# Performance work log

Hardware: AMD Instinct MI355X
Metric: run time of the kernel (lower is better)

Reference implementation:

```python
import jax, jax.numpy as jnp
import numpy as np

N_NODES = 100000
N_EDGES = 1600000
IN_DIM = 128
HID = 128
OUT_DIM = 64
EPS = 1e-8


def setup_inputs() -> dict:
    key = jax.random.key(0)
    ks = jax.random.split(key, 10)
    x = jax.random.normal(ks[0], (N_NODES, IN_DIM), dtype=jnp.float32)
    edge_index = jax.random.randint(ks[1], (2, N_EDGES), 0, N_NODES, dtype=jnp.int64)
    edge_attr = jax.random.uniform(ks[2], (N_EDGES, 4), dtype=jnp.float32)
    s1 = 1.0 / np.sqrt(IN_DIM)
    s2 = 1.0 / np.sqrt(HID)
    sr = 1.0 / np.sqrt(2 * HID)
    W1 = jax.random.normal(ks[3], (HID, IN_DIM), dtype=jnp.float32) * s1
    b1 = jnp.zeros((HID,), dtype=jnp.float32)
    W2 = jax.random.normal(ks[4], (HID, HID), dtype=jnp.float32) * s2
    b2 = jnp.zeros((HID,), dtype=jnp.float32)
    Wr = jax.random.normal(ks[5], (OUT_DIM, 2 * HID), dtype=jnp.float32) * sr
    br = jnp.zeros((OUT_DIM,), dtype=jnp.float32)
    return {"x": x, "edge_index": edge_index, "edge_attr": edge_attr,
            "W1": W1, "b1": b1, "W2": W2, "b2": b2, "Wr": Wr, "br": br}


def _edge_weight_from_attr_auto(edge_attr):
    # mean over features, min-max normalize, invert, clamp >= 0
    m = edge_attr.mean(axis=-1)                      # [E]
    m_min, m_max = m.min(), m.max()
    m_norm = (m - m_min) / (m_max - m_min + EPS)
    w = jnp.where(m_max - m_min > EPS, 1.0 - m_norm, jnp.ones_like(m))
    return jnp.clip(w, 0.0)


def reference(x, edge_index, edge_attr, W1, b1, W2, b2, Wr, br):
    N = x.shape[0]
    row, col = edge_index[0], edge_index[1]          # source -> target
    ew = _edge_weight_from_attr_auto(edge_attr)      # [E]
    # GCN normalization with self-loops (self-loop weight = 1.0)
    deg = jax.ops.segment_sum(ew, col, num_segments=N) + 1.0   # [N]
    dis = jax.lax.rsqrt(deg)                         # deg >= 1
    norm = dis[row] * ew * dis[col]                  # [E]

    def gcn(h, W, b):
        hW = h @ W.T                                 # [N, d_out]
        agg = jax.ops.segment_sum(norm[:, None] * hW[row], col, num_segments=N)
        # self-loop contribution: dis[i] * 1.0 * dis[i] * hW[i]
        return agg + (dis * dis)[:, None] * hW + b

    # dropout in eval mode -> identity
    h1 = jax.nn.relu(gcn(x, W1, b1))                 # [N, HID]
    h2 = jax.nn.relu(gcn(h1, W2, b2))                # [N, HID]
    hcat = jnp.concatenate([h1, h2], axis=-1)        # [N, 2*HID] (JK concat)
    return hcat @ Wr.T + br                          # residue-level [N, OUT_DIM]
```

## Files before the change

### kernel.cpp

```cpp
#include <hip/hip_runtime.h>

#define NN 100000
#define NE 1600000
#define HID 128
#define ODIM 64
#define NBK 196
#define BSHIFT 9
#define BGRID 512
#define CVTB 48
#define CHUNK 3125
#define BITER 13
#define BINCAP 12288
#define SMAX 4504
#define LMAX 568

typedef unsigned int u32;
typedef unsigned short u16;
typedef __bf16 bf16x8 __attribute__((ext_vector_type(8)));
typedef float f32x4 __attribute__((ext_vector_type(4)));
typedef float f32x2 __attribute__((ext_vector_type(2)));

__device__ __forceinline__ float bf_lo(u32 p){ return __uint_as_float(p << 16); }
__device__ __forceinline__ float bf_hi(u32 p){ return __uint_as_float(p & 0xffff0000u); }
__device__ __forceinline__ u16 f2bf(float f){
  u32 u = __float_as_uint(f);
  u += 0x7fffu + ((u >> 16) & 1u);
  return (u16)(u >> 16);
}
__device__ __forceinline__ bf16x8 ld8bf(const u16* p){ return *(const bf16x8*)p; }
__device__ __forceinline__ bf16x8 cvt8(const float* p){
  union { bf16x8 v; u16 s[8]; } r;
#pragma unroll
  for (int i = 0; i < 8; i++) r.s[i] = f2bf(p[i]);
  return r.v;
}

__global__ __launch_bounds__(256) void k_bin(
    const float* __restrict__ eattr, const int* __restrict__ erow,
    const int* __restrict__ ecol, u32* __restrict__ bcur,
    uint2* __restrict__ bin, u32* __restrict__ minmax,
    const float* __restrict__ W1, const float* __restrict__ W2,
    const float* __restrict__ Wr, u16* __restrict__ W1b,
    u16* __restrict__ W2b, u16* __restrict__ Wrb){
  int tid = threadIdx.x;
  if (blockIdx.x >= BGRID){
    int i = (blockIdx.x - BGRID) * 256 + tid;
    const float* src; u16* dst; int off;
    if (i < 4096){ src = W1; dst = W1b; off = i; }
    else if (i < 8192){ src = W2; dst = W2b; off = i - 4096; }
    else { src = Wr; dst = Wrb; off = i - 8192; }
    float4 v = ((const float4*)src)[off];
    uint2 o;
    o.x = (u32)f2bf(v.x) | ((u32)f2bf(v.y) << 16);
    o.y = (u32)f2bf(v.z) | ((u32)f2bf(v.w) << 16);
    ((uint2*)dst)[off] = o;
    return;
  }
  __shared__ u32 lcnt4[4 * NBK], wof4[4 * NBK];
  __shared__ u32 lofs[NBK], gb[NBK];
  __shared__ u32 scn[256];
  __shared__ u16 lmap[LMAX];
  __shared__ uint2 stage[SMAX];
  __shared__ u32 Tt;
  __shared__ float smin[4], smax[4];
  for (int t = tid; t < 4 * NBK; t += 256) lcnt4[t] = 0;
  __syncthreads();
  int base = blockIdx.x * CHUNK;
  int wid = tid >> 6, lane = tid & 63;
  float lmin = __uint_as_float(0x7f800000u), lmax = 0.f;
  u32 pk[BITER]; float mv[BITER]; u32 sv[BITER];
#pragma unroll
  for (int it = 0; it < BITER; it++){
    int idx = it * 256 + tid;
    u32 p = 0xFFFFFFFFu; float m = 0.f; u32 s = 0;
    if (idx < CHUNK){
      int e = base + idx;
      float4 a = ((const float4*)eattr)[e];
      m = 0.25f * (a.x + a.y + a.z + a.w);
      lmin = fminf(lmin, m); lmax = fmaxf(lmax, m);
      int c = ecol[e];
      s = (u32)erow[e]; if (s >= NN) s = 0;
      if ((u32)c < NN){
        u32 b = (u32)c >> BSHIFT;
        u32 r = atomicAdd(&lcnt4[wid * NBK + b], 1u);
        p = (b << 21) | (((u32)c & 511u) << 12) | r;
      }
    }
    pk[it] = p; mv[it] = m; sv[it] = s;
  }
  __syncthreads();
  u32 na = 0, n = 0;
  if (tid < NBK){
    u32 n0 = lcnt4[tid], n1 = lcnt4[NBK + tid];
    u32 n2 = lcnt4[2 * NBK + tid], n3 = lcnt4[3 * NBK + tid];
    n = n0 + n1 + n2 + n3;
    na = (n + 7u) & ~7u;
    wof4[tid] = 0; wof4[NBK + tid] = n0;
    wof4[2 * NBK + tid] = n0 + n1; wof4[3 * NBK + tid] = n0 + n1 + n2;
  }
  scn[tid] = na; __syncthreads();
  for (int s = 1; s < 256; s <<= 1){
    u32 t = (tid >= s) ? scn[tid - s] : 0;
    __syncthreads();
    scn[tid] += t;
    __syncthreads();
  }
  u32 ex = scn[tid] - na;
  if (tid < NBK){
    lofs[tid] = ex;
    u32 g = 0x80000000u;
    if (na){
      u32 gl = atomicAdd(&bcur[tid], na);
      if (gl + na <= BINCAP) g = (u32)tid * BINCAP + gl;
    }
    gb[tid] = g;
    for (u32 l = ex >> 3; l < (ex + na) >> 3; l++) lmap[l] = (u16)tid;
    uint2 sent; sent.x = 0xFFFFFFFFu; sent.y = 0u;
    for (u32 k = n; k < na; k++) stage[ex + k] = sent;
  }
  if (tid == 255) Tt = scn[255];
  __syncthreads();
#pragma unroll
  for (int it = 0; it < BITER; it++){
    u32 p = pk[it];
    if (p == 0xFFFFFFFFu) continue;
    u32 b = p >> 21;
    uint2 rec; rec.x = sv[it] | (((p >> 12) & 511u) << 17); rec.y = __float_as_uint(mv[it]);
    stage[lofs[b] + wof4[wid * NBK + b] + (p & 4095u)] = rec;
  }
  __syncthreads();
  u32 T = Tt;
  for (u32 i = tid; i < T; i += 256){
    u32 b = lmap[i >> 3];
    u32 g = gb[b];
    if (g != 0x80000000u) bin[g + (i - lofs[b])] = stage[i];
  }
  for (int off = 32; off; off >>= 1){
    lmin = fminf(lmin, __shfl_xor(lmin, off));
    lmax = fmaxf(lmax, __shfl_xor(lmax, off));
  }
  if (lane == 0){ smin[wid] = lmin; smax[wid] = lmax; }
  __syncthreads();
  if (tid == 0){
    float mn = fminf(fminf(smin[0], smin[1]), fminf(smin[2], smin[3]));
    float mx = fmaxf(fmaxf(smax[0], smax[1]), fmaxf(smax[2], smax[3]));
    atomicMax(&minmax[0], ~__float_as_uint(mn));
    atomicMax(&minmax[1], __float_as_uint(mx));
  }
}

__global__ __launch_bounds__(1024) void k_sort(
    const u32* __restrict__ bcur, const uint2* __restrict__ bin,
    const u32* __restrict__ minmax, u32* __restrict__ csr,
    u32* __restrict__ meta, float* __restrict__ dis){
  int b = blockIdx.x;
  int bb = b * BINCAP, nrec = (int)bcur[b];
  float mn  = __uint_as_float(~minmax[0]);
  float mx  = __uint_as_float(minmax[1]);
  float rng = mx - mn;
  bool flat = !(rng > 1e-8f);
  float inv = 1.f / (rng + 1e-8f);
  __shared__ u32 cnt[512], off[512], cur[512], degfx[512];
  __shared__ uint2 sbin[BINCAP];
  int tid = threadIdx.x;
  if (tid < 512){ cnt[tid] = 0; degfx[tid] = 0; }
  __syncthreads();
  for (int i = tid; i < nrec; i += 1024){
    uint2 r = bin[bb + i];
    uint2 srec; srec.x = 0xFFFFFFFFu; srec.y = 0u;
    if (r.x != 0xFFFFFFFFu){
      u32 d = (r.x >> 17) & 511u;
      float w = flat ? 1.f : fmaxf(1.f - (__uint_as_float(r.y) - mn) * inv, 0.f);
      atomicAdd(&cnt[d], 1u);
      atomicAdd(&degfx[d], (u32)(w * 1048576.f + 0.5f));
      srec.x = (r.x & 0x1FFFFu) | ((u32)(w * 32767.f + 0.5f) << 17);
      srec.y = d;
    }
    sbin[i] = srec;
  }
  __syncthreads();
  u32 v = 0;
  if (tid < 512){ v = cnt[tid]; off[tid] = v; }
  __syncthreads();
  for (int s = 1; s < 512; s <<= 1){
    u32 t = 0;
    if (tid < 512 && tid >= s) t = off[tid - s];
    __syncthreads();
    if (tid < 512) off[tid] += t;
    __syncthreads();
  }
  if (tid < 512){
    u32 ex = off[tid] - v;
    cur[tid] = ex;
    int node = (b << BSHIFT) + tid;
    if (node < NN){
      meta[node] = ((u32)bb + ex) | (v << 22);
      dis[node] = rsqrtf(1.f + (float)degfx[tid] * (1.f / 1048576.f));
    }
  }
  __syncthreads();
  for (int i = tid; i < nrec; i += 1024){
    uint2 s = sbin[i];
    if (s.x == 0xFFFFFFFFu) continue;
    u32 pos = (u32)bb + atomicAdd(&cur[s.y], 1u);
    csr[pos] = s.x;
  }
}

template <bool A_F32>
__global__ __launch_bounds__(256) void k_gemm128(
    const void* __restrict__ Av, const u16* __restrict__ Bt,
    const float* __restrict__ dis, u16* __restrict__ G){
  int wave = threadIdx.x >> 6, lane = threadIdx.x & 63;
  int m0 = blockIdx.x * 32;
  int m = lane & 15, q = lane >> 4;
  const float* a0f = (const float*)Av + (size_t)(m0 + m) * HID;
  const float* a1f = a0f + (size_t)16 * HID;
  const u16*   a0b = (const u16*)Av   + (size_t)(m0 + m) * HID;
  const u16*   a1b = a0b + (size_t)16 * HID;
  const u16* brow0 = Bt + (size_t)(wave * 16 + m) * HID;
  const u16* brow1 = brow0 + (size_t)64 * HID;
  f32x4 acc00 = {0.f,0.f,0.f,0.f}, acc01 = {0.f,0.f,0.f,0.f};
  f32x4 acc10 = {0.f,0.f,0.f,0.f}, acc11 = {0.f,0.f,0.f,0.f};
#pragma unroll
  for (int kb = 0; kb < HID; kb += 32){
    bf16x8 af0 = A_F32 ? cvt8(a0f + kb + q * 8) : ld8bf(a0b + kb + q * 8);
    bf16x8 af1 = A_F32 ? cvt8(a1f + kb + q * 8) : ld8bf(a1b + kb + q * 8);
    bf16x8 bf0 = ld8bf(brow0 + kb + q * 8);
    bf16x8 bf1 = ld8bf(brow1 + kb + q * 8);
    acc00 = __builtin_amdgcn_mfma_f32_16x16x32_bf16(af0, bf0, acc00, 0, 0, 0);
    acc01 = __builtin_amdgcn_mfma_f32_16x16x32_bf16(af0, bf1, acc01, 0, 0, 0);
    acc10 = __builtin_amdgcn_mfma_f32_16x16x32_bf16(af1, bf0, acc10, 0, 0, 0);
    acc11 = __builtin_amdgcn_mfma_f32_16x16x32_bf16(af1, bf1, acc11, 0, 0, 0);
  }
  u16* crow0 = G + (size_t)(m0 + q * 4) * HID + wave * 16 + m;
  u16* crow1 = crow0 + (size_t)16 * HID;
#pragma unroll
  for (int r = 0; r < 4; r++){
    float d0 = dis[m0 + q * 4 + r];
    float d1 = dis[m0 + 16 + q * 4 + r];
    crow0[(size_t)r * HID]      = f2bf(acc00[r] * d0);
    crow0[(size_t)r * HID + 64] = f2bf(acc01[r] * d0);
    crow1[(size_t)r * HID]      = f2bf(acc10[r] * d1);
    crow1[(size_t)r * HID + 64] = f2bf(acc11[r] * d1);
  }
}

__global__ __launch_bounds__(256) void k_aggregate(
    const u32* __restrict__ meta, const u32* __restrict__ csr,
    const float* __restrict__ dis, const u16* __restrict__ g,
    const float* __restrict__ bias, u16* __restrict__ hout){
  int node = __builtin_amdgcn_readfirstlane(
      (int)(blockIdx.x * 4 + (threadIdx.x >> 6)));
  int lane = threadIdx.x & 63;
  const u32* gp = (const u32*)g;
  u32 sv = gp[((size_t)node << 6) + lane];
  u32 mw = meta[node];
  float di = dis[node];
  u32 s = mw & 0x3FFFFFu;
  int c = (int)(mw >> 22);
  const u32* cp = csr + s;
  f32x2 acc = {0.f, 0.f};
  int j = 0;
  for (; j + 16 <= c; j += 16){
    u32 p[16];
#pragma unroll
    for (int t = 0; t < 16; t++)
      p[t] = __builtin_amdgcn_readfirstlane(cp[j + t]);
    u32 pv[16];
#pragma unroll
    for (int t = 0; t < 16; t++)
      pv[t] = gp[(size_t)(p[t] & 0x1FFFFu) * 64u + lane];
#pragma unroll
    for (int t = 0; t < 16; t++){
      float wf = (float)(p[t] >> 17);
      f32x2 val = {bf_lo(pv[t]), bf_hi(pv[t])};
      f32x2 w2 = {wf, wf};
      acc += w2 * val;
    }
  }
  for (; j < c; j += 8){
    u32 p[8];
#pragma unroll
    for (int t = 0; t < 8; t++)
      p[t] = __builtin_amdgcn_readfirstlane(cp[j + t]);
    u32 st[8]; u32 wi[8];
#pragma unroll
    for (int t = 0; t < 8; t++){
      bool ok = (j + t) < c;
      st[t] = ok ? (p[t] & 0x1FFFFu) : 0u;
      wi[t] = ok ? (p[t] >> 17) : 0u;
    }
    u32 pv[8];
#pragma unroll
    for (int t = 0; t < 8; t++)
      pv[t] = gp[(size_t)st[t] * 64u + lane];
#pragma unroll
    for (int t = 0; t < 8; t++){
      float wf = (float)wi[t];
      f32x2 val = {bf_lo(pv[t]), bf_hi(pv[t])};
      f32x2 w2 = {wf, wf};
      acc += w2 * val;
    }
  }
  float2 bv = ((const float2*)bias)[lane];
  f32x2 selfv = {bf_lo(sv), bf_hi(sv)};
  float d2 = di * (1.f / 32767.f);
  float o0 = fmaxf(acc.x * d2 + (selfv.x * di + bv.x), 0.f);
  float o1 = fmaxf(acc.y * d2 + (selfv.y * di + bv.y), 0.f);
  ((u32*)hout)[((size_t)node << 6) + lane] = (u32)f2bf(o0) | ((u32)f2bf(o1) << 16);
}

__global__ __launch_bounds__(256) void k_readout(
    const u16* __restrict__ h1, const u16* __restrict__ h2,
    const u16* __restrict__ Wrb, const float* __restrict__ br, float* __restrict__ out){
  int wave = threadIdx.x >> 6, lane = threadIdx.x & 63;
  int m0 = blockIdx.x * 32;
  int n0 = wave * 16;
  int m = lane & 15, q = lane >> 4;
  const u16* a10 = h1 + (size_t)(m0 + m) * HID;
  const u16* a11 = a10 + (size_t)16 * HID;
  const u16* a20 = h2 + (size_t)(m0 + m) * HID;
  const u16* a21 = a20 + (size_t)16 * HID;
  const u16* b  = Wrb + (size_t)(n0 + m) * (2 * HID);
  f32x4 acc0 = {0.f,0.f,0.f,0.f}, acc1 = {0.f,0.f,0.f,0.f};
#pragma unroll
  for (int kb = 0; kb < HID; kb += 32){
    bf16x8 bf = ld8bf(b + kb + q * 8);
    acc0 = __builtin_amdgcn_mfma_f32_16x16x32_bf16(ld8bf(a10 + kb + q * 8), bf, acc0, 0, 0, 0);
    acc1 = __builtin_amdgcn_mfma_f32_16x16x32_bf16(ld8bf(a11 + kb + q * 8), bf, acc1, 0, 0, 0);
  }
#pragma unroll
  for (int kb = 0; kb < HID; kb += 32){
    bf16x8 bf = ld8bf(b + HID + kb + q * 8);
    acc0 = __builtin_amdgcn_mfma_f32_16x16x32_bf16(ld8bf(a20 + kb + q * 8), bf, acc0, 0, 0, 0);
    acc1 = __builtin_amdgcn_mfma_f32_16x16x32_bf16(ld8bf(a21 + kb + q * 8), bf, acc1, 0, 0, 0);
  }
  float bias = br[n0 + m];
  float* crow0 = out + (size_t)(m0 + q * 4) * ODIM + n0 + m;
  float* crow1 = crow0 + (size_t)16 * ODIM;
#pragma unroll
  for (int r = 0; r < 4; r++){
    crow0[(size_t)r * ODIM] = acc0[r] + bias;
    crow1[(size_t)r * ODIM] = acc1[r] + bias;
  }
}

extern "C" void kernel_launch(void* const* d_in, const int* in_sizes, int n_in,
                              void* d_out, int out_size, void* d_ws, size_t ws_size,
                              hipStream_t stream){
  const float* x     = (const float*)d_in[0];
  const int*   eidx  = (const int*)d_in[1];
  const float* eattr = (const float*)d_in[2];
  const float* W1    = (const float*)d_in[3];
  const float* b1    = (const float*)d_in[4];
  const float* W2    = (const float*)d_in[5];
  const float* b2    = (const float*)d_in[6];
  const float* Wr    = (const float*)d_in[7];
  const float* br    = (const float*)d_in[8];
  const int* erow  = eidx;
  const int* ecol  = eidx + NE;

  char* w = (char*)d_ws;
  auto carve = [&](size_t bytes) -> void* {
    void* p = (void*)w;
    w += (bytes + 255) & ~(size_t)255;
    return p;
  };
  u32* csr       = (u32*)carve((size_t)NBK * BINCAP * 4);
  u32* bcur      = (u32*)carve(256 * 4);
  u32* minmax    = (u32*)carve(256);
  u32* meta      = (u32*)carve((size_t)NN * 4);
  float* dis     = (float*)carve((size_t)NN * 4);
  u16* W1b       = (u16*)carve((size_t)HID * HID * 2);
  u16* W2b       = (u16*)carve((size_t)HID * HID * 2);
  u16* Wrb       = (u16*)carve((size_t)ODIM * 2 * HID * 2);
  u16* g         = (u16*)carve((size_t)NN * HID * 2);
  u16* h1        = (u16*)carve((size_t)NN * HID * 2);
  u16* h2        = (u16*)carve((size_t)NN * HID * 2);
  uint2* bin     = (uint2*)h2;

  hipMemsetAsync(bcur, 0, 1024 + 256, stream);
  k_bin<<<BGRID + CVTB, 256, 0, stream>>>(eattr, erow, ecol, bcur, bin, minmax,
                                          W1, W2, Wr, W1b, W2b, Wrb);
  k_sort<<<NBK, 1024, 0, stream>>>(bcur, bin, minmax, csr, meta, dis);

  k_gemm128<true><<<NN / 32, 256, 0, stream>>>(x, W1b, dis, g);
  k_aggregate<<<NN / 4, 256, 0, stream>>>(meta, csr, dis, g, b1, h1);
  k_gemm128<false><<<NN / 32, 256, 0, stream>>>(h1, W2b, dis, g);
  k_aggregate<<<NN / 4, 256, 0, stream>>>(meta, csr, dis, g, b2, h2);
  k_readout<<<NN / 32, 256, 0, stream>>>(h1, h2, Wrb, br, (float*)d_out);
}
```

Measured before the change: 381.5 us.

## Replace binned LDS sort with global-atomic count, scan, and scatter CSR build

The two-stage bucket-binning and shared-memory sort that built the CSR is replaced by three simpler kernels. The first counts in-degree per node with global atomics and stores the per-edge attribute mean. The second scans the counts per 512-node bucket, and the third scatters edges into the CSR with global atomic cursors while accumulating fixed-point degree. The stored dis array is removed and recomputed from degfx wherever it is used. This trades the heavy shared-memory staging for about 3.2M random global atomics and an extra pass over the edge arrays. Edge order within each node's list also becomes nondeterministic.

```diff
diff --git a/kernel.cpp b/kernel.cpp
--- a/kernel.cpp
+++ b/kernel.cpp
@@ -6,13 +6,10 @@
 #define ODIM 64
 #define NBK 196
 #define BSHIFT 9
-#define BGRID 512
+#define BINCAP 12288
+#define P1B 1024
 #define CVTB 48
-#define CHUNK 3125
-#define BITER 13
-#define BINCAP 12288
-#define SMAX 4504
-#define LMAX 568
+#define P2B 2048
 
 typedef unsigned int u32;
 typedef unsigned short u16;
@@ -34,17 +31,19 @@
   for (int i = 0; i < 8; i++) r.s[i] = f2bf(p[i]);
   return r.v;
 }
-
-__global__ __launch_bounds__(256) void k_bin(
-    const float* __restrict__ eattr, const int* __restrict__ erow,
-    const int* __restrict__ ecol, u32* __restrict__ bcur,
-    uint2* __restrict__ bin, u32* __restrict__ minmax,
+__device__ __forceinline__ float deg2dis(u32 dfx){
+  return rsqrtf(1.f + (float)dfx * (1.f / 1048576.f));
+}
+
+__global__ __launch_bounds__(256) void k_p1(
+    const float* __restrict__ eattr, const int* __restrict__ ecol,
+    u32* __restrict__ cnt, float* __restrict__ marr, u32* __restrict__ minmax,
     const float* __restrict__ W1, const float* __restrict__ W2,
     const float* __restrict__ Wr, u16* __restrict__ W1b,
     u16* __restrict__ W2b, u16* __restrict__ Wrb){
   int tid = threadIdx.x;
-  if (blockIdx.x >= BGRID){
-    int i = (blockIdx.x - BGRID) * 256 + tid;
+  if (blockIdx.x >= P1B){
+    int i = (blockIdx.x - P1B) * 256 + tid;
     const float* src; u16* dst; int off;
     if (i < 4096){ src = W1; dst = W1b; off = i; }
     else if (i < 8192){ src = W2; dst = W2b; off = i - 4096; }
@@ -56,84 +55,16 @@
     ((uint2*)dst)[off] = o;
     return;
   }
-  __shared__ u32 lcnt4[4 * NBK], wof4[4 * NBK];
-  __shared__ u32 lofs[NBK], gb[NBK];
-  __shared__ u32 scn[256];
-  __shared__ u16 lmap[LMAX];
-  __shared__ uint2 stage[SMAX];
-  __shared__ u32 Tt;
   __shared__ float smin[4], smax[4];
-  for (int t = tid; t < 4 * NBK; t += 256) lcnt4[t] = 0;
-  __syncthreads();
-  int base = blockIdx.x * CHUNK;
   int wid = tid >> 6, lane = tid & 63;
   float lmin = __uint_as_float(0x7f800000u), lmax = 0.f;
-  u32 pk[BITER]; float mv[BITER]; u32 sv[BITER];
-#pragma unroll
-  for (int it = 0; it < BITER; it++){
-    int idx = it * 256 + tid;
-    u32 p = 0xFFFFFFFFu; float m = 0.f; u32 s = 0;
-    if (idx < CHUNK){
-      int e = base + idx;
-      float4 a = ((const float4*)eattr)[e];
-      m = 0.25f * (a.x + a.y + a.z + a.w);
-      lmin = fminf(lmin, m); lmax = fmaxf(lmax, m);
-      int c = ecol[e];
-      s = (u32)erow[e]; if (s >= NN) s = 0;
-      if ((u32)c < NN){
-        u32 b = (u32)c >> BSHIFT;
-        u32 r = atomicAdd(&lcnt4[wid * NBK + b], 1u);
-        p = (b << 21) | (((u32)c & 511u) << 12) | r;
-      }
-    }
-    pk[it] = p; mv[it] = m; sv[it] = s;
-  }
-  __syncthreads();
-  u32 na = 0, n = 0;
-  if (tid < NBK){
-    u32 n0 = lcnt4[tid], n1 = lcnt4[NBK + tid];
-    u32 n2 = lcnt4[2 * NBK + tid], n3 = lcnt4[3 * NBK + tid];
-    n = n0 + n1 + n2 + n3;
-    na = (n + 7u) & ~7u;
-    wof4[tid] = 0; wof4[NBK + tid] = n0;
-    wof4[2 * NBK + tid] = n0 + n1; wof4[3 * NBK + tid] = n0 + n1 + n2;
-  }
-  scn[tid] = na; __syncthreads();
-  for (int s = 1; s < 256; s <<= 1){
-    u32 t = (tid >= s) ? scn[tid - s] : 0;
-    __syncthreads();
-    scn[tid] += t;
-    __syncthreads();
-  }
-  u32 ex = scn[tid] - na;
-  if (tid < NBK){
-    lofs[tid] = ex;
-    u32 g = 0x80000000u;
-    if (na){
-      u32 gl = atomicAdd(&bcur[tid], na);
-      if (gl + na <= BINCAP) g = (u32)tid * BINCAP + gl;
-    }
-    gb[tid] = g;
-    for (u32 l = ex >> 3; l < (ex + na) >> 3; l++) lmap[l] = (u16)tid;
-    uint2 sent; sent.x = 0xFFFFFFFFu; sent.y = 0u;
-    for (u32 k = n; k < na; k++) stage[ex + k] = sent;
-  }
-  if (tid == 255) Tt = scn[255];
-  __syncthreads();
-#pragma unroll
-  for (int it = 0; it < BITER; it++){
-    u32 p = pk[it];
-    if (p == 0xFFFFFFFFu) continue;
-    u32 b = p >> 21;
-    uint2 rec; rec.x = sv[it] | (((p >> 12) & 511u) << 17); rec.y = __float_as_uint(mv[it]);
-    stage[lofs[b] + wof4[wid * NBK + b] + (p & 4095u)] = rec;
-  }
-  __syncthreads();
-  u32 T = Tt;
-  for (u32 i = tid; i < T; i += 256){
-    u32 b = lmap[i >> 3];
-    u32 g = gb[b];
-    if (g != 0x80000000u) bin[g + (i - lofs[b])] = stage[i];
+  for (int e = blockIdx.x * 256 + tid; e < NE; e += P1B * 256){
+    float4 a = ((const float4*)eattr)[e];
+    float m = 0.25f * (a.x + a.y + a.z + a.w);
+    marr[e] = m;
+    lmin = fminf(lmin, m); lmax = fmaxf(lmax, m);
+    u32 c = (u32)ecol[e];
+    if (c < NN) atomicAdd(&cnt[c], 1u);
   }
   for (int off = 32; off; off >>= 1){
     lmin = fminf(lmin, __shfl_xor(lmin, off));
@@ -149,68 +80,51 @@
   }
 }
 
-__global__ __launch_bounds__(1024) void k_sort(
-    const u32* __restrict__ bcur, const uint2* __restrict__ bin,
-    const u32* __restrict__ minmax, u32* __restrict__ csr,
-    u32* __restrict__ meta, float* __restrict__ dis){
-  int b = blockIdx.x;
-  int bb = b * BINCAP, nrec = (int)bcur[b];
+__global__ __launch_bounds__(512) void k_scan(
+    const u32* __restrict__ cnt, u32* __restrict__ meta, u32* __restrict__ cur){
+  __shared__ u32 sc[512];
+  int b = blockIdx.x, tid = threadIdx.x;
+  int node = (b << BSHIFT) + tid;
+  u32 v = (node < NN) ? cnt[node] : 0u;
+  sc[tid] = v; __syncthreads();
+  for (int s = 1; s < 512; s <<= 1){
+    u32 t = (tid >= s) ? sc[tid - s] : 0u;
+    __syncthreads();
+    sc[tid] += t;
+    __syncthreads();
+  }
+  u32 rs = (u32)(b * BINCAP) + (sc[tid] - v);
+  if (node < NN){
+    meta[node] = rs | (v << 22);
+    cur[node] = rs;
+  }
+}
+
+__global__ __launch_bounds__(256) void k_p2(
+    const float* __restrict__ marr, const int* __restrict__ erow,
+    const int* __restrict__ ecol, const u32* __restrict__ minmax,
+    u32* __restrict__ cur, u32* __restrict__ csr, u32* __restrict__ degfx){
   float mn  = __uint_as_float(~minmax[0]);
   float mx  = __uint_as_float(minmax[1]);
   float rng = mx - mn;
   bool flat = !(rng > 1e-8f);
   float inv = 1.f / (rng + 1e-8f);
-  __shared__ u32 cnt[512], off[512], cur[512], degfx[512];
-  __shared__ uint2 sbin[BINCAP];
-  int tid = threadIdx.x;
-  if (tid < 512){ cnt[tid] = 0; degfx[tid] = 0; }
-  __syncthreads();
-  for (int i = tid; i < nrec; i += 1024){
-    uint2 r = bin[bb + i];
-    uint2 srec; srec.x = 0xFFFFFFFFu; srec.y = 0u;
-    if (r.x != 0xFFFFFFFFu){
-      u32 d = (r.x >> 17) & 511u;
-      float w = flat ? 1.f : fmaxf(1.f - (__uint_as_float(r.y) - mn) * inv, 0.f);
-      atomicAdd(&cnt[d], 1u);
-      atomicAdd(&degfx[d], (u32)(w * 1048576.f + 0.5f));
-      srec.x = (r.x & 0x1FFFFu) | ((u32)(w * 32767.f + 0.5f) << 17);
-      srec.y = d;
-    }
-    sbin[i] = srec;
-  }
-  __syncthreads();
-  u32 v = 0;
-  if (tid < 512){ v = cnt[tid]; off[tid] = v; }
-  __syncthreads();
-  for (int s = 1; s < 512; s <<= 1){
-    u32 t = 0;
-    if (tid < 512 && tid >= s) t = off[tid - s];
-    __syncthreads();
-    if (tid < 512) off[tid] += t;
-    __syncthreads();
-  }
-  if (tid < 512){
-    u32 ex = off[tid] - v;
-    cur[tid] = ex;
-    int node = (b << BSHIFT) + tid;
-    if (node < NN){
-      meta[node] = ((u32)bb + ex) | (v << 22);
-      dis[node] = rsqrtf(1.f + (float)degfx[tid] * (1.f / 1048576.f));
-    }
-  }
-  __syncthreads();
-  for (int i = tid; i < nrec; i += 1024){
-    uint2 s = sbin[i];
-    if (s.x == 0xFFFFFFFFu) continue;
-    u32 pos = (u32)bb + atomicAdd(&cur[s.y], 1u);
-    csr[pos] = s.x;
+  for (int e = blockIdx.x * 256 + threadIdx.x; e < NE; e += P2B * 256){
+    float m = marr[e];
+    u32 c = (u32)ecol[e];
+    u32 s = (u32)erow[e]; if (s >= NN) s = 0;
+    if (c >= NN) continue;
+    float w = flat ? 1.f : fmaxf(1.f - (m - mn) * inv, 0.f);
+    u32 pos = atomicAdd(&cur[c], 1u);
+    csr[pos] = s | ((u32)(w * 32767.f + 0.5f) << 17);
+    atomicAdd(&degfx[c], (u32)(w * 1048576.f + 0.5f));
   }
 }
 
 template <bool A_F32>
 __global__ __launch_bounds__(256) void k_gemm128(
     const void* __restrict__ Av, const u16* __restrict__ Bt,
-    const float* __restrict__ dis, u16* __restrict__ G){
+    const u32* __restrict__ degfx, u16* __restrict__ G){
   int wave = threadIdx.x >> 6, lane = threadIdx.x & 63;
   int m0 = blockIdx.x * 32;
   int m = lane & 15, q = lane >> 4;
@@ -237,8 +151,8 @@
   u16* crow1 = crow0 + (size_t)16 * HID;
 #pragma unroll
   for (int r = 0; r < 4; r++){
-    float d0 = dis[m0 + q * 4 + r];
-    float d1 = dis[m0 + 16 + q * 4 + r];
+    float d0 = deg2dis(degfx[m0 + q * 4 + r]);
+    float d1 = deg2dis(degfx[m0 + 16 + q * 4 + r]);
     crow0[(size_t)r * HID]      = f2bf(acc00[r] * d0);
     crow0[(size_t)r * HID + 64] = f2bf(acc01[r] * d0);
     crow1[(size_t)r * HID]      = f2bf(acc10[r] * d1);
@@ -248,7 +162,7 @@
 
 __global__ __launch_bounds__(256) void k_aggregate(
     const u32* __restrict__ meta, const u32* __restrict__ csr,
-    const float* __restrict__ dis, const u16* __restrict__ g,
+    const u32* __restrict__ degfx, const u16* __restrict__ g,
     const float* __restrict__ bias, u16* __restrict__ hout){
   int node = __builtin_amdgcn_readfirstlane(
       (int)(blockIdx.x * 4 + (threadIdx.x >> 6)));
@@ -256,7 +170,7 @@
   const u32* gp = (const u32*)g;
   u32 sv = gp[((size_t)node << 6) + lane];
   u32 mw = meta[node];
-  float di = dis[node];
+  float di = deg2dis(degfx[node]);
   u32 s = mw & 0x3FFFFFu;
   int c = (int)(mw >> 22);
   const u32* cp = csr + s;
@@ -368,26 +282,29 @@
     return p;
   };
   u32* csr       = (u32*)carve((size_t)NBK * BINCAP * 4);
-  u32* bcur      = (u32*)carve(256 * 4);
+  u32* cnt       = (u32*)carve((size_t)NN * 4);
+  u32* degfx     = (u32*)carve((size_t)NN * 4);
   u32* minmax    = (u32*)carve(256);
+  u32* cur       = (u32*)carve((size_t)NN * 4);
   u32* meta      = (u32*)carve((size_t)NN * 4);
-  float* dis     = (float*)carve((size_t)NN * 4);
   u16* W1b       = (u16*)carve((size_t)HID * HID * 2);
   u16* W2b       = (u16*)carve((size_t)HID * HID * 2);
   u16* Wrb       = (u16*)carve((size_t)ODIM * 2 * HID * 2);
   u16* g         = (u16*)carve((size_t)NN * HID * 2);
   u16* h1        = (u16*)carve((size_t)NN * HID * 2);
   u16* h2        = (u16*)carve((size_t)NN * HID * 2);
-  uint2* bin     = (uint2*)h2;
-
-  hipMemsetAsync(bcur, 0, 1024 + 256, stream);
-  k_bin<<<BGRID + CVTB, 256, 0, stream>>>(eattr, erow, ecol, bcur, bin, minmax,
-                                          W1, W2, Wr, W1b, W2b, Wrb);
-  k_sort<<<NBK, 1024, 0, stream>>>(bcur, bin, minmax, csr, meta, dis);
-
-  k_gemm128<true><<<NN / 32, 256, 0, stream>>>(x, W1b, dis, g);
-  k_aggregate<<<NN / 4, 256, 0, stream>>>(meta, csr, dis, g, b1, h1);
-  k_gemm128<false><<<NN / 32, 256, 0, stream>>>(h1, W2b, dis, g);
-  k_aggregate<<<NN / 4, 256, 0, stream>>>(meta, csr, dis, g, b2, h2);
+  float* marr    = (float*)g;
+
+  size_t zspan = (size_t)((char*)minmax + 256 - (char*)cnt);
+  hipMemsetAsync(cnt, 0, zspan, stream);
+  k_p1<<<P1B + CVTB, 256, 0, stream>>>(eattr, ecol, cnt, marr, minmax,
+                                       W1, W2, Wr, W1b, W2b, Wrb);
+  k_scan<<<NBK, 512, 0, stream>>>(cnt, meta, cur);
+  k_p2<<<P2B, 256, 0, stream>>>(marr, erow, ecol, minmax, cur, csr, degfx);
+
+  k_gemm128<true><<<NN / 32, 256, 0, stream>>>(x, W1b, degfx, g);
+  k_aggregate<<<NN / 4, 256, 0, stream>>>(meta, csr, degfx, g, b1, h1);
+  k_gemm128<false><<<NN / 32, 256, 0, stream>>>(h1, W2b, degfx, g);
+  k_aggregate<<<NN / 4, 256, 0, stream>>>(meta, csr, degfx, g, b2, h2);
   k_readout<<<NN / 32, 256, 0, stream>>>(h1, h2, Wrb, br, (float*)d_out);
 }
```

After: 567.1 us. +48.7%, slower.

## Split bucket sort into global-count scan and scatter kernels, dropping LDS staging

Applied to the files above, without the earlier changes.

Per-node in-degree counts move into k_bin as global atomics, a new k_scan kernel builds CSR offsets with wave shuffles, and k_scatter writes CSR entries directly instead of staging 12288 records in LDS and running a block-wide scan. The aim is to get rid of the large shared-memory buffer, which limits occupancy, and the serialized scan barriers in the old sort kernel. The cost is 1.6M extra global atomics in k_bin, one more kernel launch, and a larger memset. CSR order within a node becomes nondeterministic, which may slightly change floating-point summation order.

```diff
diff --git a/kernel.cpp b/kernel.cpp
--- a/kernel.cpp
+++ b/kernel.cpp
@@ -38,7 +38,7 @@
 __global__ __launch_bounds__(256) void k_bin(
     const float* __restrict__ eattr, const int* __restrict__ erow,
     const int* __restrict__ ecol, u32* __restrict__ bcur,
-    uint2* __restrict__ bin, u32* __restrict__ minmax,
+    uint2* __restrict__ bin, u32* __restrict__ minmax, u32* __restrict__ cnt,
     const float* __restrict__ W1, const float* __restrict__ W2,
     const float* __restrict__ Wr, u16* __restrict__ W1b,
     u16* __restrict__ W2b, u16* __restrict__ Wrb){
@@ -84,6 +84,7 @@
         u32 b = (u32)c >> BSHIFT;
         u32 r = atomicAdd(&lcnt4[wid * NBK + b], 1u);
         p = (b << 21) | (((u32)c & 511u) << 12) | r;
+        atomicAdd(&cnt[c], 1u);
       }
     }
     pk[it] = p; mv[it] = m; sv[it] = s;
@@ -149,61 +150,62 @@
   }
 }
 
-__global__ __launch_bounds__(1024) void k_sort(
+__global__ __launch_bounds__(512) void k_scan(
+    const u32* __restrict__ cnt, u32* __restrict__ meta, u32* __restrict__ cur){
+  __shared__ u32 wtot[8];
+  int b = blockIdx.x, tid = threadIdx.x;
+  int wid = tid >> 6, lane = tid & 63;
+  int node = (b << BSHIFT) + tid;
+  u32 v = (node < NN) ? cnt[node] : 0u;
+  u32 incl = v;
+  for (int off = 1; off < 64; off <<= 1){
+    u32 t = (u32)__shfl_up((int)incl, off);
+    if (lane >= off) incl += t;
+  }
+  if (lane == 63) wtot[wid] = incl;
+  __syncthreads();
+  u32 pre = 0;
+#pragma unroll
+  for (int k = 0; k < 8; k++) pre += (k < wid) ? wtot[k] : 0u;
+  u32 rs = (u32)(b * BINCAP) + pre + incl - v;
+  if (node < NN){
+    meta[node] = rs | (v << 22);
+    cur[node] = rs;
+  }
+}
+
+__global__ __launch_bounds__(1024) void k_scatter(
     const u32* __restrict__ bcur, const uint2* __restrict__ bin,
-    const u32* __restrict__ minmax, u32* __restrict__ csr,
-    u32* __restrict__ meta, float* __restrict__ dis){
-  int b = blockIdx.x;
-  int bb = b * BINCAP, nrec = (int)bcur[b];
+    const u32* __restrict__ minmax, const u32* __restrict__ cur,
+    u32* __restrict__ csr, float* __restrict__ dis){
+  __shared__ u32 curL[512], degL[512];
+  int b = blockIdx.x, tid = threadIdx.x;
+  int bb = b * BINCAP;
+  int nrec = (int)min(bcur[b], (u32)BINCAP);
+  if (tid < 512){
+    int node = (b << BSHIFT) + tid;
+    curL[tid] = (node < NN) ? cur[node] : 0u;
+    degL[tid] = 0u;
+  }
+  __syncthreads();
   float mn  = __uint_as_float(~minmax[0]);
   float mx  = __uint_as_float(minmax[1]);
   float rng = mx - mn;
   bool flat = !(rng > 1e-8f);
   float inv = 1.f / (rng + 1e-8f);
-  __shared__ u32 cnt[512], off[512], cur[512], degfx[512];
-  __shared__ uint2 sbin[BINCAP];
-  int tid = threadIdx.x;
-  if (tid < 512){ cnt[tid] = 0; degfx[tid] = 0; }
-  __syncthreads();
   for (int i = tid; i < nrec; i += 1024){
     uint2 r = bin[bb + i];
-    uint2 srec; srec.x = 0xFFFFFFFFu; srec.y = 0u;
-    if (r.x != 0xFFFFFFFFu){
-      u32 d = (r.x >> 17) & 511u;
-      float w = flat ? 1.f : fmaxf(1.f - (__uint_as_float(r.y) - mn) * inv, 0.f);
-      atomicAdd(&cnt[d], 1u);
-      atomicAdd(&degfx[d], (u32)(w * 1048576.f + 0.5f));
-      srec.x = (r.x & 0x1FFFFu) | ((u32)(w * 32767.f + 0.5f) << 17);
-      srec.y = d;
-    }
-    sbin[i] = srec;
-  }
-  __syncthreads();
-  u32 v = 0;
-  if (tid < 512){ v = cnt[tid]; off[tid] = v; }
-  __syncthreads();
-  for (int s = 1; s < 512; s <<= 1){
-    u32 t = 0;
-    if (tid < 512 && tid >= s) t = off[tid - s];
-    __syncthreads();
-    if (tid < 512) off[tid] += t;
-    __syncthreads();
-  }
+    if (r.x == 0xFFFFFFFFu) continue;
+    u32 d = (r.x >> 17) & 511u;
+    float w = flat ? 1.f : fmaxf(1.f - (__uint_as_float(r.y) - mn) * inv, 0.f);
+    u32 pos = atomicAdd(&curL[d], 1u);
+    csr[pos] = (r.x & 0x1FFFFu) | ((u32)(w * 32767.f + 0.5f) << 17);
+    atomicAdd(&degL[d], (u32)(w * 1048576.f + 0.5f));
+  }
+  __syncthreads();
   if (tid < 512){
-    u32 ex = off[tid] - v;
-    cur[tid] = ex;
     int node = (b << BSHIFT) + tid;
-    if (node < NN){
-      meta[node] = ((u32)bb + ex) | (v << 22);
-      dis[node] = rsqrtf(1.f + (float)degfx[tid] * (1.f / 1048576.f));
-    }
-  }
-  __syncthreads();
-  for (int i = tid; i < nrec; i += 1024){
-    uint2 s = sbin[i];
-    if (s.x == 0xFFFFFFFFu) continue;
-    u32 pos = (u32)bb + atomicAdd(&cur[s.y], 1u);
-    csr[pos] = s.x;
+    if (node < NN) dis[node] = rsqrtf(1.f + (float)degL[tid] * (1.f / 1048576.f));
   }
 }
 
@@ -370,6 +372,8 @@
   u32* csr       = (u32*)carve((size_t)NBK * BINCAP * 4);
   u32* bcur      = (u32*)carve(256 * 4);
   u32* minmax    = (u32*)carve(256);
+  u32* cnt       = (u32*)carve((size_t)NN * 4);
+  u32* cur       = (u32*)carve((size_t)NN * 4);
   u32* meta      = (u32*)carve((size_t)NN * 4);
   float* dis     = (float*)carve((size_t)NN * 4);
   u16* W1b       = (u16*)carve((size_t)HID * HID * 2);
@@ -380,10 +384,12 @@
   u16* h2        = (u16*)carve((size_t)NN * HID * 2);
   uint2* bin     = (uint2*)h2;
 
-  hipMemsetAsync(bcur, 0, 1024 + 256, stream);
+  size_t zspan = (size_t)((char*)cnt + (size_t)NN * 4 - (char*)bcur);
+  hipMemsetAsync(bcur, 0, zspan, stream);
   k_bin<<<BGRID + CVTB, 256, 0, stream>>>(eattr, erow, ecol, bcur, bin, minmax,
-                                          W1, W2, Wr, W1b, W2b, Wrb);
-  k_sort<<<NBK, 1024, 0, stream>>>(bcur, bin, minmax, csr, meta, dis);
+                                          cnt, W1, W2, Wr, W1b, W2b, Wrb);
+  k_scan<<<NBK, 512, 0, stream>>>(cnt, meta, cur);
+  k_scatter<<<NBK, 1024, 0, stream>>>(bcur, bin, minmax, cur, csr, dis);
 
   k_gemm128<true><<<NN / 32, 256, 0, stream>>>(x, W1b, dis, g);
   k_aggregate<<<NN / 4, 256, 0, stream>>>(meta, csr, dis, g, b1, h1);
```

Measured after the change: 429.0 us. +12.4%, slower.
